# Kernel optimization log

Hardware: AMD Instinct MI355X
Metric: run time of the kernel (lower is better)

Reference implementation:

```python
import jax, jax.numpy as jnp
import numpy as np

DIM, QK, PDIM = 384, 16, 96
EPS = 1e-5

def _bn(x, w, b, m, v):
    # eval-mode BatchNorm2d over channel axis 1 of [B,C,H,W]
    inv = w / jnp.sqrt(v + EPS)
    return x * inv[:, None, None] + (b - m * inv)[:, None, None]

def setup_inputs() -> dict:
    key = jax.random.key(0)
    ks = jax.random.split(key, 12)
    B, H, W = 64, 32, 32
    out_qkv = 2 * QK + PDIM  # 128
    return {
        "x": jax.random.normal(ks[0], (B, DIM, H, W), jnp.float32),
        "gn_w": jax.random.normal(ks[1], (PDIM,), jnp.float32) * 0.1 + 1.0,
        "gn_b": jax.random.normal(ks[2], (PDIM,), jnp.float32) * 0.1,
        "qkv_w": jax.random.normal(ks[3], (out_qkv, PDIM), jnp.float32) * 0.1,
        "qkv_bn_w": jax.random.normal(ks[4], (out_qkv,), jnp.float32) * 0.1 + 1.0,
        "qkv_bn_b": jax.random.normal(ks[5], (out_qkv,), jnp.float32) * 0.1,
        "qkv_bn_m": jax.random.normal(ks[6], (out_qkv,), jnp.float32) * 0.1,
        "qkv_bn_v": jax.random.uniform(ks[7], (out_qkv,), jnp.float32, 0.5, 1.5),
        "proj_w": jax.random.normal(ks[8], (DIM, DIM), jnp.float32) * 0.05,
        "proj_bn_w": jax.random.normal(ks[9], (DIM,), jnp.float32) * 0.1 + 1.0,
        "proj_bn_b": jax.random.normal(ks[10], (DIM,), jnp.float32) * 0.1,
        "proj_bn_m": jax.random.normal(ks[11], (DIM,), jnp.float32) * 0.1,
        "proj_bn_v": jax.random.uniform(jax.random.fold_in(key, 99), (DIM,), jnp.float32, 0.5, 1.5),
    }

def reference(x, gn_w, gn_b, qkv_w, qkv_bn_w, qkv_bn_b, qkv_bn_m, qkv_bn_v,
              proj_w, proj_bn_w, proj_bn_b, proj_bn_m, proj_bn_v):
    B, C, H, W = x.shape
    N = H * W
    scale = QK ** -0.5
    x1, x2 = x[:, :PDIM], x[:, PDIM:]
    # GroupNorm with 1 group: normalize over (C,H,W) per sample, per-channel affine
    mu = jnp.mean(x1, axis=(1, 2, 3), keepdims=True)
    var = jnp.var(x1, axis=(1, 2, 3), keepdims=True)
    x1n = (x1 - mu) * jax.lax.rsqrt(var + EPS)
    x1n = x1n * gn_w[:, None, None] + gn_b[:, None, None]
    # 1x1 conv (no bias) + eval BN
    qkv = jnp.einsum('oc,bchw->bohw', qkv_w, x1n)
    qkv = _bn(qkv, qkv_bn_w, qkv_bn_b, qkv_bn_m, qkv_bn_v)
    q = qkv[:, :QK].reshape(B, QK, N)
    k = qkv[:, QK:2 * QK].reshape(B, QK, N)
    v = qkv[:, 2 * QK:].reshape(B, PDIM, N)
    attn = jnp.einsum('bcn,bcm->bnm', q, k) * scale      # [B,N,N]
    attn = jax.nn.softmax(attn, axis=-1)
    x1o = jnp.einsum('bcm,bnm->bcn', v, attn).reshape(B, PDIM, H, W)
    y = jax.nn.silu(jnp.concatenate([x1o, x2], axis=1))
    y = jnp.einsum('oc,bchw->bohw', proj_w, y)
    return _bn(y, proj_bn_w, proj_bn_b, proj_bn_m, proj_bn_v)
```

## Files before the change

### kernel.cpp

```cpp
#include <hip/hip_runtime.h>

#define EPS 1e-5f

constexpr int B   = 64;
constexpr int DIM = 384;
constexpr int PD  = 96;
constexpr int QKD = 16;
constexpr int N   = 1024;
constexpr int OQ  = 128;
constexpr int Y2C = DIM - PD;
constexpr int VST = 72;
#define QSCALE 0.3606737602222408f

typedef __attribute__((ext_vector_type(8))) short bf16x8;
typedef __attribute__((ext_vector_type(16))) float f32x16;

#define MFMA(a, b, c) __builtin_amdgcn_mfma_f32_32x32x16_bf16((a), (b), (c), 0, 0, 0)

#define GLOAD16(gsrc, ldst)                                                    \
    __builtin_amdgcn_global_load_lds(                                          \
        (const __attribute__((address_space(1))) void*)(gsrc),                 \
        (__attribute__((address_space(3))) void*)(ldst), 16, 0, 0)

__device__ __forceinline__ unsigned short f2bf(float f) {
    union { float f; unsigned u; } v; v.f = f;
    unsigned r = v.u + 0x7fffu + ((v.u >> 16) & 1u);
    return (unsigned short)(r >> 16);
}
__device__ __forceinline__ unsigned pack2(float a, float b) {
    return (unsigned)f2bf(a) | ((unsigned)f2bf(b) << 16);
}
__device__ __forceinline__ unsigned cvtpk(float lo, float hi_) {
    unsigned r;
    asm("v_cvt_pk_bf16_f32 %0, %1, %2" : "=v"(r) : "v"(lo), "v"(hi_));
    return r;
}
__device__ __forceinline__ float max3f(float a, float b, float c) {
    return fmaxf(fmaxf(a, b), c);
}
__device__ __forceinline__ f32x16 zero16() {
    f32x16 z;
#pragma unroll
    for (int i = 0; i < 16; i++) z[i] = 0.f;
    return z;
}

__global__ __launch_bounds__(256) void k_pre(const float* __restrict__ x,
                                             float* __restrict__ part,
                                             const float* __restrict__ pw,
                                             const float* __restrict__ pbnw,
                                             const float* __restrict__ pbnb,
                                             const float* __restrict__ pbnm,
                                             const float* __restrict__ pbnv,
                                             short* __restrict__ Wp,
                                             float* __restrict__ bias,
                                             const float* __restrict__ qw,
                                             const float* __restrict__ qbnw,
                                             const float* __restrict__ qbnb,
                                             const float* __restrict__ qbnm,
                                             const float* __restrict__ qbnv,
                                             short* __restrict__ Wq,
                                             float* __restrict__ qbias) {
    __shared__ float r1[4], r2[4];
    int gb = blockIdx.x;
    int tid = threadIdx.x;
    if (gb < 512) {
        int b = gb >> 3, p = gb & 7;
        const float4* xp = (const float4*)(x + (size_t)b * DIM * N) + p * 3072;
        float s1a = 0.f, s1b = 0.f, s1c = 0.f, s1d = 0.f;
        float s2a = 0.f, s2b = 0.f, s2c = 0.f, s2d = 0.f;
        #pragma unroll
        for (int i = 0; i < 12; i += 4) {
            float4 v0 = xp[tid + (i + 0) * 256];
            float4 v1 = xp[tid + (i + 1) * 256];
            float4 v2 = xp[tid + (i + 2) * 256];
            float4 v3 = xp[tid + (i + 3) * 256];
            s1a += v0.x + v0.y + v0.z + v0.w;
            s2a += v0.x * v0.x + v0.y * v0.y + v0.z * v0.z + v0.w * v0.w;
            s1b += v1.x + v1.y + v1.z + v1.w;
            s2b += v1.x * v1.x + v1.y * v1.y + v1.z * v1.z + v1.w * v1.w;
            s1c += v2.x + v2.y + v2.z + v2.w;
            s2c += v2.x * v2.x + v2.y * v2.y + v2.z * v2.z + v2.w * v2.w;
            s1d += v3.x + v3.y + v3.z + v3.w;
            s2d += v3.x * v3.x + v3.y * v3.y + v3.z * v3.z + v3.w * v3.w;
        }
        float s1 = (s1a + s1b) + (s1c + s1d);
        float s2 = (s2a + s2b) + (s2c + s2d);
        for (int o = 32; o > 0; o >>= 1) {
            s1 += __shfl_down(s1, o, 64);
            s2 += __shfl_down(s2, o, 64);
        }
        int wave = tid >> 6, lane = tid & 63;
        if (lane == 0) { r1[wave] = s1; r2[wave] = s2; }
        __syncthreads();
        if (tid == 0) {
            part[(b * 8 + p) * 2 + 0] = r1[0] + r1[1] + r1[2] + r1[3];
            part[(b * 8 + p) * 2 + 1] = r2[0] + r2[1] + r2[2] + r2[3];
        }
    } else if (gb < 512 + 576) {
        int idx = (gb - 512) * 256 + tid;
        int o = idx / DIM;
        float inv = pbnw[o] * rsqrtf(pbnv[o] + EPS);
        Wp[idx] = (short)f2bf(pw[idx] * inv);
        if (idx < DIM) bias[idx] = pbnb[idx] - pbnm[idx] * (pbnw[idx] * rsqrtf(pbnv[idx] + EPS));
    } else {
        int idx = (gb - 1088) * 256 + tid;
        int o = idx / PD;
        float inv = qbnw[o] * rsqrtf(qbnv[o] + EPS);
        float f = (o < QKD) ? QSCALE : 1.f;
        Wq[idx] = (short)f2bf(qw[idx] * inv * f);
        if (idx < OQ) {
            float invb = qbnw[idx] * rsqrtf(qbnv[idx] + EPS);
            float fb = (idx < QKD) ? QSCALE : 1.f;
            qbias[idx] = (qbnb[idx] - qbnm[idx] * invb) * fb;
        }
    }
}

__global__ __launch_bounds__(256) void k_qkv(const float* __restrict__ x,
                                             const float* __restrict__ part,
                                             const float* __restrict__ gnw,
                                             const float* __restrict__ gnb,
                                             const short* __restrict__ Wq,
                                             const float* __restrict__ qbias,
                                             short* __restrict__ Qt,
                                             short* __restrict__ Kt,
                                             short* __restrict__ Vw) {
    alignas(16) __shared__ short Wl[128 * 104];
    alignas(16) __shared__ short Xl[128 * 104];
    __shared__ short t[32][132];
    __shared__ float qbl[OQ];
    __shared__ float pr[16];
    int b = blockIdx.x, nb = blockIdx.y;
    int tid = threadIdx.x, w = tid >> 6, l = tid & 63;
    int col = l & 31, hi = l >> 5;
    int wr = w >> 1, wc = w & 1;
    int n0 = nb * 128;

    if (tid < 16) pr[tid] = part[b * 16 + tid];
    if (tid >= 64 && tid < 64 + OQ) qbl[tid - 64] = qbias[tid - 64];
    #pragma unroll
    for (int it = 0; it < 6; it++) {
        int e = tid + 256 * it;
        int row = e / 12, slot = e % 12;
        *(uint4*)&Wl[row * 104 + slot * 8] = *(const uint4*)(Wq + row * PD + slot * 8);
    }
    __syncthreads();
    float s1 = (pr[0] + pr[2]) + (pr[4] + pr[6]) + (pr[8] + pr[10]) + (pr[12] + pr[14]);
    float s2 = (pr[1] + pr[3]) + (pr[5] + pr[7]) + (pr[9] + pr[11]) + (pr[13] + pr[15]);
    float mu = s1 / (PD * N);
    float var = s2 / (PD * N) - mu * mu;
    float rsig = rsqrtf(var + EPS);

    const float* xb = x + (size_t)b * DIM * N + n0;
    for (int ct = 0; ct < 3; ct++) {
        int c0 = ct * 32;
        if (ct) __syncthreads();
        #pragma unroll
        for (int i = 0; i < 4; i++) {
            int e = tid + 256 * i;
            int c = e >> 5, q4 = e & 31;
            float4 v = *(const float4*)(xb + (size_t)(c0 + c) * N + q4 * 4);
            float s = rsig * gnw[c0 + c];
            float tt = gnb[c0 + c] - mu * s;
            uint2 d;
            d.x = pack2(s * v.x + tt, s * v.y + tt);
            d.y = pack2(s * v.z + tt, s * v.w + tt);
            *(uint2*)&t[c][q4 * 4] = d;
        }
        __syncthreads();
        #pragma unroll
        for (int i = 0; i < 8; i++) {
            int e = tid + 256 * i;
            int n = e >> 4, cp = e & 15;
            unsigned lo = (unsigned short)t[2 * cp][n];
            unsigned hi2 = (unsigned short)t[2 * cp + 1][n];
            *(unsigned*)&Xl[n * 104 + c0 + 2 * cp] = lo | (hi2 << 16);
        }
    }
    __syncthreads();

    f32x16 acc[2][2];
    acc[0][0] = zero16(); acc[0][1] = zero16();
    acc[1][0] = zero16(); acc[1][1] = zero16();
    #pragma unroll
    for (int ks = 0; ks < 6; ks++) {
        int ko = ks * 16 + hi * 8;
        int ra0 = wr * 64 + col, ra1 = ra0 + 32;
        int rb0 = wc * 64 + col, rb1 = rb0 + 32;
        bf16x8 a0 = *(const bf16x8*)&Wl[ra0 * 104 + ko];
        bf16x8 a1 = *(const bf16x8*)&Wl[ra1 * 104 + ko];
        bf16x8 b0 = *(const bf16x8*)&Xl[rb0 * 104 + ko];
        bf16x8 b1 = *(const bf16x8*)&Xl[rb1 * 104 + ko];
        acc[0][0] = MFMA(a0, b0, acc[0][0]);
        acc[0][1] = MFMA(a0, b1, acc[0][1]);
        acc[1][0] = MFMA(a1, b0, acc[1][0]);
        acc[1][1] = MFMA(a1, b1, acc[1][1]);
    }

    #pragma unroll
    for (int m = 0; m < 2; m++) {
        int o_base = wr * 64 + m * 32;
        #pragma unroll
        for (int nn = 0; nn < 2; nn++) {
            int n = n0 + wc * 64 + nn * 32 + col;
            f32x16 a = acc[m][nn];
            if (o_base == 0) {
                #pragma unroll
                for (int g = 0; g < 4; g++) {
                    int ofr = 8 * g + 4 * hi;
                    float v0 = a[4 * g + 0] + qbl[ofr + 0];
                    float v1 = a[4 * g + 1] + qbl[ofr + 1];
                    float v2 = a[4 * g + 2] + qbl[ofr + 2];
                    float v3 = a[4 * g + 3] + qbl[ofr + 3];
                    uint2 d; d.x = pack2(v0, v1); d.y = pack2(v2, v3);
                    short* dst = (g < 2)
                        ? (Qt + ((size_t)b * N + n) * QKD + (ofr & 15))
                        : (Kt + ((size_t)b * N + n) * QKD + (ofr & 15));
                    *(uint2*)dst = d;
                }
            } else {
                int c0 = o_base - 32;
                int np = (n & ~12) | ((n & 4) << 1) | ((n & 8) >> 1);
                short* vb = Vw + ((size_t)b * PD + c0) * N + np;
                #pragma unroll
                for (int r = 0; r < 16; r++) {
                    int cf = (r & 3) + 8 * (r >> 2) + 4 * hi;
                    vb[(size_t)cf * N] = (short)f2bf(a[r] + qbl[32 + c0 + cf]);
                }
            }
        }
    }
}

__global__ __launch_bounds__(512, 2) void k_attn(const short* __restrict__ Qt,
                                                 const short* __restrict__ Kt,
                                                 const short* __restrict__ Vb,
                                                 short* __restrict__ y1t) {
    alignas(16) __shared__ char lds_raw[4 * 96 * VST * 2];
    short* Vs = (short*)lds_raw;
    float* combA_ = (float*)lds_raw;
    float* combM_ = (float*)(lds_raw + 50176);
    float* combL_ = (float*)(lds_raw + 51200);

    int b = blockIdx.x;
    int tid = threadIdx.x;
    int split = tid >> 8;
    int s_tid = tid & 255;
    int w = tid >> 6, lane = tid & 63;
    int qgrp = w & 3;
    int col = lane & 31, hi = lane >> 5;
    int q0 = blockIdx.y * 128 + qgrp * 32;
    int kbeg = split * 512;

    const short* kbase = Kt + (size_t)b * N * QKD;
    const short* vbase = Vb + (size_t)b * PD * N;
    const bf16x8 qf = *(const bf16x8*)(Qt + ((size_t)b * N + q0 + col) * QKD + hi * 8);

    short* vs0 = Vs + (split * 2 + 0) * (96 * VST);
    short* vs1 = Vs + (split * 2 + 1) * (96 * VST);

    bf16x8 kf0 = *(const bf16x8*)(kbase + (size_t)(kbeg + col) * QKD + hi * 8);
    bf16x8 kf1 = *(const bf16x8*)(kbase + (size_t)(kbeg + 32 + col) * QKD + hi * 8);
    {
        int t0 = s_tid, t1 = s_tid + 256, t2i = s_tid + 512;
        uint4 g0 = *(const uint4*)(vbase + (size_t)(t0 >> 3) * N + kbeg + (t0 & 7) * 8);
        uint4 g1 = *(const uint4*)(vbase + (size_t)(t1 >> 3) * N + kbeg + (t1 & 7) * 8);
        uint4 g2 = *(const uint4*)(vbase + (size_t)(t2i >> 3) * N + kbeg + (t2i & 7) * 8);
        *(uint4*)(vs0 + (t0 >> 3) * VST + (t0 & 7) * 8) = g0;
        *(uint4*)(vs0 + (t1 >> 3) * VST + (t1 & 7) * 8) = g1;
        *(uint4*)(vs0 + (t2i >> 3) * VST + (t2i & 7) * 8) = g2;
    }
    __syncthreads();

    f32x16 acc0 = zero16(), acc1 = zero16(), acc2 = zero16();
    float m = -1e30f, lsum = 0.f;

    for (int it = 0; it < 8; it++) {
        int m0 = kbeg + it * 64;
        short* cur = (it & 1) ? vs1 : vs0;
        short* nxt = (it & 1) ? vs0 : vs1;
        bool more = (it < 7);
        int m0n = more ? m0 + 64 : m0;
        bf16x8 kf0n = *(const bf16x8*)(kbase + (size_t)(m0n + col) * QKD + hi * 8);
        bf16x8 kf1n = *(const bf16x8*)(kbase + (size_t)(m0n + 32 + col) * QKD + hi * 8);
        uint4 g0, g1, g2;
        if (more) {
            int t0 = s_tid, t1 = s_tid + 256, t2i = s_tid + 512;
            g0 = *(const uint4*)(vbase + (size_t)(t0 >> 3) * N + m0n + (t0 & 7) * 8);
            g1 = *(const uint4*)(vbase + (size_t)(t1 >> 3) * N + m0n + (t1 & 7) * 8);
            g2 = *(const uint4*)(vbase + (size_t)(t2i >> 3) * N + m0n + (t2i & 7) * 8);
        }

        f32x16 s0 = MFMA(kf0, qf, zero16());
        f32x16 s1 = MFMA(kf1, qf, zero16());
        float a0 = max3f(s0[0], s0[1], s0[2]),  a1 = max3f(s0[3], s0[4], s0[5]);
        float a2 = max3f(s0[6], s0[7], s0[8]),  a3 = max3f(s0[9], s0[10], s0[11]);
        float a4 = max3f(s0[12], s0[13], s0[14]);
        float cm0 = fmaxf(max3f(a0, a1, a2), max3f(a3, a4, s0[15]));
        float b0_ = max3f(s1[0], s1[1], s1[2]),  b1_ = max3f(s1[3], s1[4], s1[5]);
        float b2_ = max3f(s1[6], s1[7], s1[8]),  b3_ = max3f(s1[9], s1[10], s1[11]);
        float b4_ = max3f(s1[12], s1[13], s1[14]);
        float cm1 = fmaxf(max3f(b0_, b1_, b2_), max3f(b3_, b4_, s1[15]));
        float cm = fmaxf(cm0, cm1);
        cm = fmaxf(cm, __shfl_xor(cm, 32, 64));
        if (!__all(cm <= m + 8.f)) {
            float mnew = fmaxf(m, cm);
            float corr = __builtin_amdgcn_exp2f(m - mnew);
            m = mnew;
            lsum *= corr;
            #pragma unroll
            for (int r = 0; r < 16; r++) { acc0[r] *= corr; acc1[r] *= corr; acc2[r] *= corr; }
        }
        float ps = 0.f;
        bf16x8 pbv[2][2];
        #pragma unroll
        for (int s32 = 0; s32 < 2; s32++) {
            const f32x16& s = s32 ? s1 : s0;
            unsigned pw[8];
            #pragma unroll
            for (int j = 0; j < 8; j++) {
                float p0 = __builtin_amdgcn_exp2f(s[2 * j] - m);
                float p1 = __builtin_amdgcn_exp2f(s[2 * j + 1] - m);
                ps += p0 + p1;
                pw[j] = cvtpk(p0, p1);
            }
            union { unsigned u[4]; bf16x8 v; } pb0, pb1;
            pb0.u[0] = pw[0]; pb0.u[1] = pw[1]; pb0.u[2] = pw[2]; pb0.u[3] = pw[3];
            pb1.u[0] = pw[4]; pb1.u[1] = pw[5]; pb1.u[2] = pw[6]; pb1.u[3] = pw[7];
            pbv[s32][0] = pb0.v;
            pbv[s32][1] = pb1.v;
        }
        ps += __shfl_xor(ps, 32, 64);
        lsum += ps;
        __builtin_amdgcn_s_setprio(1);
        #pragma unroll
        for (int s32 = 0; s32 < 2; s32++) {
            const short* vt32 = cur + s32 * 32 + hi * 8;
            bf16x8 pa = pbv[s32][0], pq = pbv[s32][1];
            bf16x8 va0 = *(const bf16x8*)(vt32 + col * VST);
            bf16x8 va1 = *(const bf16x8*)(vt32 + col * VST + 16);
            acc0 = MFMA(va0, pa, acc0);
            acc0 = MFMA(va1, pq, acc0);
            bf16x8 vb0 = *(const bf16x8*)(vt32 + (32 + col) * VST);
            bf16x8 vb1 = *(const bf16x8*)(vt32 + (32 + col) * VST + 16);
            acc1 = MFMA(vb0, pa, acc1);
            acc1 = MFMA(vb1, pq, acc1);
            bf16x8 vc0 = *(const bf16x8*)(vt32 + (64 + col) * VST);
            bf16x8 vc1 = *(const bf16x8*)(vt32 + (64 + col) * VST + 16);
            acc2 = MFMA(vc0, pa, acc2);
            acc2 = MFMA(vc1, pq, acc2);
        }
        __builtin_amdgcn_s_setprio(0);
        kf0 = kf0n; kf1 = kf1n;
        if (more) {
            int t0 = s_tid, t1 = s_tid + 256, t2i = s_tid + 512;
            *(uint4*)(nxt + (t0 >> 3) * VST + (t0 & 7) * 8) = g0;
            *(uint4*)(nxt + (t1 >> 3) * VST + (t1 & 7) * 8) = g1;
            *(uint4*)(nxt + (t2i >> 3) * VST + (t2i & 7) * 8) = g2;
            __syncthreads();
        }
    }

    __syncthreads();
    if (split == 1) {
        float* dst = combA_ + (qgrp * 64 + lane) * 49;
        #pragma unroll
        for (int r = 0; r < 16; r++) {
            dst[r] = acc0[r]; dst[16 + r] = acc1[r]; dst[32 + r] = acc2[r];
        }
        combM_[qgrp * 64 + lane] = m;
        combL_[qgrp * 64 + lane] = lsum;
    }
    __syncthreads();
    if (split == 0) {
        float m2 = combM_[qgrp * 64 + lane], l2 = combL_[qgrp * 64 + lane];
        float M  = fmaxf(m, m2);
        float c1 = __builtin_amdgcn_exp2f(m - M);
        float c2 = __builtin_amdgcn_exp2f(m2 - M);
        float inv = 1.f / (lsum * c1 + l2 * c2);
        const float* src = combA_ + (qgrp * 64 + lane) * 49;
        float f1 = c1 * inv, f2 = c2 * inv;
        short* yrow = y1t + ((size_t)b * N + q0 + col) * PD;
        #pragma unroll
        for (int cg = 0; cg < 3; cg++) {
            f32x16 a = (cg == 0) ? acc0 : ((cg == 1) ? acc1 : acc2);
            const float* sr = src + cg * 16;
            #pragma unroll
            for (int j = 0; j < 8; j++) {
                float v0 = a[2 * j] * f1 + sr[2 * j] * f2;
                float v1 = a[2 * j + 1] * f1 + sr[2 * j + 1] * f2;
                v0 = v0 / (1.f + __expf(-v0));
                v1 = v1 / (1.f + __expf(-v1));
                int c = cg * 32 + ((2 * j) & 3) + 8 * (j >> 1) + 4 * hi;
                *(unsigned*)(yrow + c) = pack2(v0, v1);
            }
        }
    }
}

__global__ __launch_bounds__(256) void k_trans(const float* __restrict__ x,
                                               short* __restrict__ y2t) {
    int b = blockIdx.x, ct = blockIdx.y, nt = blockIdx.z;
    int tid = threadIdx.x;
    __shared__ short t[32][132];
    int c0 = PD + ct * 32, n0 = nt * 128;
    const float* xb = x + ((size_t)b * DIM + c0) * N + n0;
    #pragma unroll
    for (int i = 0; i < 4; i++) {
        int e = tid + 256 * i;
        int c = e >> 5, q4 = e & 31;
        float4 v = *(const float4*)(xb + (size_t)c * N + q4 * 4);
        float s0 = v.x / (1.f + __expf(-v.x));
        float s1 = v.y / (1.f + __expf(-v.y));
        float s2 = v.z / (1.f + __expf(-v.z));
        float s3 = v.w / (1.f + __expf(-v.w));
        uint2 d;
        d.x = pack2(s0, s1);
        d.y = pack2(s2, s3);
        *(uint2*)&t[c][q4 * 4] = d;
    }
    __syncthreads();
    #pragma unroll
    for (int i = 0; i < 8; i++) {
        int e = tid + 256 * i;
        int n = e >> 4, cp = e & 15;
        unsigned lo = (unsigned short)t[2 * cp][n];
        unsigned hi = (unsigned short)t[2 * cp + 1][n];
        *(unsigned*)(y2t + ((size_t)b * N + n0 + n) * Y2C + ct * 32 + 2 * cp) = lo | (hi << 16);
    }
}

__global__ __launch_bounds__(256) void k_proj(const short* __restrict__ Wp,
                                              const short* __restrict__ y1t,
                                              const short* __restrict__ y2t,
                                              const float* __restrict__ bias,
                                              float* __restrict__ out) {
    __shared__ short Asl[128 * 32];
    __shared__ short Bsl[128 * 32];
    int b = blockIdx.x, ob = blockIdx.y, nb = blockIdx.z;
    int tid = threadIdx.x, w = tid >> 6, l = tid & 63;
    int col = l & 31, hi = l >> 5;
    int wr = w >> 1, wc = w & 1;
    int o0 = ob * 128, n0 = nb * 128;
    size_t bn = (size_t)b * N + n0;

    f32x16 acc[2][2];
    acc[0][0] = zero16(); acc[0][1] = zero16();
    acc[1][0] = zero16(); acc[1][1] = zero16();

    int srow = (l >> 2);
    int sslotbase = (l & 3);

    for (int step = 0; step < 12; step++) {
        int k0 = step * 32;
        const short* ysrc;
        int ystride, kq;
        if (k0 < PD) { ysrc = y1t; ystride = PD;  kq = k0; }
        else         { ysrc = y2t; ystride = Y2C; kq = k0 - PD; }
        #pragma unroll
        for (int i = 0; i < 2; i++) {
            int row = w * 32 + i * 16 + srow;
            int sl = sslotbase ^ (row & 3);
            GLOAD16(Wp + (size_t)(o0 + row) * DIM + k0 + sl * 8,
                    &Asl[(w * 32 + i * 16) * 32]);
            GLOAD16(ysrc + (bn + row) * ystride + kq + sl * 8,
                    &Bsl[(w * 32 + i * 16) * 32]);
        }
        __syncthreads();
        #pragma unroll
        for (int kh = 0; kh < 2; kh++) {
            int bxor = ((kh << 5) + (hi << 4));
            int ra0 = wr * 64 + col,      ra1 = ra0 + 32;
            int rb0 = wc * 64 + col,      rb1 = rb0 + 32;
            bf16x8 a0 = *(const bf16x8*)&Asl[ra0 * 32 + ((bxor ^ ((ra0 & 3) << 4)) >> 1)];
            bf16x8 a1 = *(const bf16x8*)&Asl[ra1 * 32 + ((bxor ^ ((ra1 & 3) << 4)) >> 1)];
            bf16x8 b0 = *(const bf16x8*)&Bsl[rb0 * 32 + ((bxor ^ ((rb0 & 3) << 4)) >> 1)];
            bf16x8 b1 = *(const bf16x8*)&Bsl[rb1 * 32 + ((bxor ^ ((rb1 & 3) << 4)) >> 1)];
            acc[0][0] = MFMA(a0, b0, acc[0][0]);
            acc[0][1] = MFMA(a0, b1, acc[0][1]);
            acc[1][0] = MFMA(a1, b0, acc[1][0]);
            acc[1][1] = MFMA(a1, b1, acc[1][1]);
        }
        __syncthreads();
    }
    #pragma unroll
    for (int m = 0; m < 2; m++) {
        #pragma unroll
        for (int n = 0; n < 2; n++) {
            #pragma unroll
            for (int r = 0; r < 16; r++) {
                int o = o0 + wr * 64 + m * 32 + (r & 3) + 8 * (r >> 2) + 4 * hi;
                out[((size_t)b * DIM + o) * N + n0 + wc * 64 + n * 32 + col] =
                    acc[m][n][r] + bias[o];
            }
        }
    }
}

extern "C" void kernel_launch(void* const* d_in, const int* in_sizes, int n_in,
                              void* d_out, int out_size, void* d_ws, size_t ws_size,
                              hipStream_t stream) {
    const float* x    = (const float*)d_in[0];
    const float* gnw  = (const float*)d_in[1];
    const float* gnb  = (const float*)d_in[2];
    const float* qkvw = (const float*)d_in[3];
    const float* qbnw = (const float*)d_in[4];
    const float* qbnb = (const float*)d_in[5];
    const float* qbnm = (const float*)d_in[6];
    const float* qbnv = (const float*)d_in[7];
    const float* pw   = (const float*)d_in[8];
    const float* pbnw = (const float*)d_in[9];
    const float* pbnb = (const float*)d_in[10];
    const float* pbnm = (const float*)d_in[11];
    const float* pbnv = (const float*)d_in[12];
    float* out = (float*)d_out;

    char* p = (char*)d_ws;
    float* part  = (float*)p;  p += 4096;
    short* Wp    = (short*)p;  p += (size_t)DIM * DIM * 2;
    float* bias  = (float*)p;  p += 1536;
    short* Wq    = (short*)p;  p += (size_t)OQ * PD * 2;
    float* qbias = (float*)p;  p += 512;
    short* y1t   = (short*)p;  p += (size_t)B * N * PD * 2;
    short* Qt    = (short*)p;
    short* Kt    = Qt + (size_t)B * N * QKD;
    short* Vw    = Kt + (size_t)B * N * QKD;
    short* y2t   = Qt;

    k_pre<<<1136, 256, 0, stream>>>(x, part, pw, pbnw, pbnb, pbnm, pbnv, Wp, bias,
                                    qkvw, qbnw, qbnb, qbnm, qbnv, Wq, qbias);
    k_qkv<<<dim3(B, 8), 256, 0, stream>>>(x, part, gnw, gnb, Wq, qbias, Qt, Kt, Vw);
    k_attn<<<dim3(B, 8), 512, 0, stream>>>(Qt, Kt, Vw, y1t);
    k_trans<<<dim3(B, 9, 8), 256, 0, stream>>>(x, y2t);
    k_proj<<<dim3(B, 3, 8), 256, 0, stream>>>(Wp, y1t, y2t, bias, out);
}
```

Baseline: 105.4 us.

## Drop split-K in attention kernel; one 256-thread block walks all keys

The attention kernel used to split the 1024 keys between two 256-thread halves of a 512-thread block and merge the two partial softmax results through LDS. Now each 256-thread block processes all 16 key tiles itself, which removes the combine step, its two extra barriers and half of the LDS buffers. Launch bounds change to 256 threads with 4 blocks per CU. The cost is half as many waves in flight on the same grid (512 blocks of 4 waves), so each wave's serial key loop is twice as long and latency hiding is reduced.

```diff
diff --git a/kernel.cpp b/kernel.cpp
--- a/kernel.cpp
+++ b/kernel.cpp
@@ -233,40 +233,33 @@
     }
 }
 
-__global__ __launch_bounds__(512, 2) void k_attn(const short* __restrict__ Qt,
+__global__ __launch_bounds__(256, 4) void k_attn(const short* __restrict__ Qt,
                                                  const short* __restrict__ Kt,
                                                  const short* __restrict__ Vb,
                                                  short* __restrict__ y1t) {
-    alignas(16) __shared__ char lds_raw[4 * 96 * VST * 2];
+    alignas(16) __shared__ char lds_raw[2 * 96 * VST * 2];
     short* Vs = (short*)lds_raw;
-    float* combA_ = (float*)lds_raw;
-    float* combM_ = (float*)(lds_raw + 50176);
-    float* combL_ = (float*)(lds_raw + 51200);
 
     int b = blockIdx.x;
     int tid = threadIdx.x;
-    int split = tid >> 8;
-    int s_tid = tid & 255;
     int w = tid >> 6, lane = tid & 63;
-    int qgrp = w & 3;
     int col = lane & 31, hi = lane >> 5;
-    int q0 = blockIdx.y * 128 + qgrp * 32;
-    int kbeg = split * 512;
+    int q0 = blockIdx.y * 128 + w * 32;
 
     const short* kbase = Kt + (size_t)b * N * QKD;
     const short* vbase = Vb + (size_t)b * PD * N;
     const bf16x8 qf = *(const bf16x8*)(Qt + ((size_t)b * N + q0 + col) * QKD + hi * 8);
 
-    short* vs0 = Vs + (split * 2 + 0) * (96 * VST);
-    short* vs1 = Vs + (split * 2 + 1) * (96 * VST);
-
-    bf16x8 kf0 = *(const bf16x8*)(kbase + (size_t)(kbeg + col) * QKD + hi * 8);
-    bf16x8 kf1 = *(const bf16x8*)(kbase + (size_t)(kbeg + 32 + col) * QKD + hi * 8);
+    short* vs0 = Vs;
+    short* vs1 = Vs + 96 * VST;
+
+    bf16x8 kf0 = *(const bf16x8*)(kbase + (size_t)(col) * QKD + hi * 8);
+    bf16x8 kf1 = *(const bf16x8*)(kbase + (size_t)(32 + col) * QKD + hi * 8);
     {
-        int t0 = s_tid, t1 = s_tid + 256, t2i = s_tid + 512;
-        uint4 g0 = *(const uint4*)(vbase + (size_t)(t0 >> 3) * N + kbeg + (t0 & 7) * 8);
-        uint4 g1 = *(const uint4*)(vbase + (size_t)(t1 >> 3) * N + kbeg + (t1 & 7) * 8);
-        uint4 g2 = *(const uint4*)(vbase + (size_t)(t2i >> 3) * N + kbeg + (t2i & 7) * 8);
+        int t0 = tid, t1 = tid + 256, t2i = tid + 512;
+        uint4 g0 = *(const uint4*)(vbase + (size_t)(t0 >> 3) * N + (t0 & 7) * 8);
+        uint4 g1 = *(const uint4*)(vbase + (size_t)(t1 >> 3) * N + (t1 & 7) * 8);
+        uint4 g2 = *(const uint4*)(vbase + (size_t)(t2i >> 3) * N + (t2i & 7) * 8);
         *(uint4*)(vs0 + (t0 >> 3) * VST + (t0 & 7) * 8) = g0;
         *(uint4*)(vs0 + (t1 >> 3) * VST + (t1 & 7) * 8) = g1;
         *(uint4*)(vs0 + (t2i >> 3) * VST + (t2i & 7) * 8) = g2;
@@ -276,17 +269,17 @@
     f32x16 acc0 = zero16(), acc1 = zero16(), acc2 = zero16();
     float m = -1e30f, lsum = 0.f;
 
-    for (int it = 0; it < 8; it++) {
-        int m0 = kbeg + it * 64;
+    for (int it = 0; it < 16; it++) {
+        int m0 = it * 64;
         short* cur = (it & 1) ? vs1 : vs0;
         short* nxt = (it & 1) ? vs0 : vs1;
-        bool more = (it < 7);
+        bool more = (it < 15);
         int m0n = more ? m0 + 64 : m0;
         bf16x8 kf0n = *(const bf16x8*)(kbase + (size_t)(m0n + col) * QKD + hi * 8);
         bf16x8 kf1n = *(const bf16x8*)(kbase + (size_t)(m0n + 32 + col) * QKD + hi * 8);
         uint4 g0, g1, g2;
         if (more) {
-            int t0 = s_tid, t1 = s_tid + 256, t2i = s_tid + 512;
+            int t0 = tid, t1 = tid + 256, t2i = tid + 512;
             g0 = *(const uint4*)(vbase + (size_t)(t0 >> 3) * N + m0n + (t0 & 7) * 8);
             g1 = *(const uint4*)(vbase + (size_t)(t1 >> 3) * N + m0n + (t1 & 7) * 8);
             g2 = *(const uint4*)(vbase + (size_t)(t2i >> 3) * N + m0n + (t2i & 7) * 8);
@@ -354,7 +347,7 @@
         __builtin_amdgcn_s_setprio(0);
         kf0 = kf0n; kf1 = kf1n;
         if (more) {
-            int t0 = s_tid, t1 = s_tid + 256, t2i = s_tid + 512;
+            int t0 = tid, t1 = tid + 256, t2i = tid + 512;
             *(uint4*)(nxt + (t0 >> 3) * VST + (t0 & 7) * 8) = g0;
             *(uint4*)(nxt + (t1 >> 3) * VST + (t1 & 7) * 8) = g1;
             *(uint4*)(nxt + (t2i >> 3) * VST + (t2i & 7) * 8) = g2;
@@ -362,39 +355,18 @@
         }
     }
 
-    __syncthreads();
-    if (split == 1) {
-        float* dst = combA_ + (qgrp * 64 + lane) * 49;
-        #pragma unroll
-        for (int r = 0; r < 16; r++) {
-            dst[r] = acc0[r]; dst[16 + r] = acc1[r]; dst[32 + r] = acc2[r];
-        }
-        combM_[qgrp * 64 + lane] = m;
-        combL_[qgrp * 64 + lane] = lsum;
-    }
-    __syncthreads();
-    if (split == 0) {
-        float m2 = combM_[qgrp * 64 + lane], l2 = combL_[qgrp * 64 + lane];
-        float M  = fmaxf(m, m2);
-        float c1 = __builtin_amdgcn_exp2f(m - M);
-        float c2 = __builtin_amdgcn_exp2f(m2 - M);
-        float inv = 1.f / (lsum * c1 + l2 * c2);
-        const float* src = combA_ + (qgrp * 64 + lane) * 49;
-        float f1 = c1 * inv, f2 = c2 * inv;
-        short* yrow = y1t + ((size_t)b * N + q0 + col) * PD;
-        #pragma unroll
-        for (int cg = 0; cg < 3; cg++) {
-            f32x16 a = (cg == 0) ? acc0 : ((cg == 1) ? acc1 : acc2);
-            const float* sr = src + cg * 16;
-            #pragma unroll
-            for (int j = 0; j < 8; j++) {
-                float v0 = a[2 * j] * f1 + sr[2 * j] * f2;
-                float v1 = a[2 * j + 1] * f1 + sr[2 * j + 1] * f2;
-                v0 = v0 / (1.f + __expf(-v0));
-                v1 = v1 / (1.f + __expf(-v1));
-                int c = cg * 32 + ((2 * j) & 3) + 8 * (j >> 1) + 4 * hi;
-                *(unsigned*)(yrow + c) = pack2(v0, v1);
-            }
+    float inv = 1.f / lsum;
+    short* yrow = y1t + ((size_t)b * N + q0 + col) * PD;
+    #pragma unroll
+    for (int cg = 0; cg < 3; cg++) {
+        f32x16 a = (cg == 0) ? acc0 : ((cg == 1) ? acc1 : acc2);
+        #pragma unroll
+        for (int j = 0; j < 8; j++) {
+            float v0 = a[2 * j] * inv, v1 = a[2 * j + 1] * inv;
+            v0 = v0 / (1.f + __expf(-v0));
+            v1 = v1 / (1.f + __expf(-v1));
+            int c = cg * 32 + ((2 * j) & 3) + 8 * (j >> 1) + 4 * hi;
+            *(unsigned*)(yrow + c) = pack2(v0, v1);
         }
     }
 }
@@ -531,7 +503,7 @@
     k_pre<<<1136, 256, 0, stream>>>(x, part, pw, pbnw, pbnb, pbnm, pbnv, Wp, bias,
                                     qkvw, qbnw, qbnb, qbnm, qbnv, Wq, qbias);
     k_qkv<<<dim3(B, 8), 256, 0, stream>>>(x, part, gnw, gnb, Wq, qbias, Qt, Kt, Vw);
-    k_attn<<<dim3(B, 8), 512, 0, stream>>>(Qt, Kt, Vw, y1t);
+    k_attn<<<dim3(B, 8), 256, 0, stream>>>(Qt, Kt, Vw, y1t);
     k_trans<<<dim3(B, 9, 8), 256, 0, stream>>>(x, y2t);
     k_proj<<<dim3(B, 3, 8), 256, 0, stream>>>(Wp, y1t, y2t, bias, out);
 }
```

Result: faster. 103.3 us (-2.0%).
